# Kernel optimization log

Measured on AMD Instinct MI355X. Metric: run time of the kernel, lower is better.

The kernel has to match this reference:

```python
import jax, jax.numpy as jnp
import numpy as np

N, E, D, R = 100000, 1600000, 64, 16


def setup_inputs() -> dict:
    key = jax.random.key(0)
    k = jax.random.split(key, 8)
    feat = jax.random.normal(k[0], (N, D), dtype=jnp.float32)
    # xavier-uniform-ish scale (gain=sqrt(2), fan_in=fan_out=D) ~ std 0.177
    relation_weight = jax.random.normal(k[1], (R, D, D), dtype=jnp.float32) * 0.17
    relation_embed = jax.random.normal(k[2], (R, D), dtype=jnp.float32)
    W1 = jax.random.normal(k[3], (D, D), dtype=jnp.float32) * 0.1
    W2 = jax.random.normal(k[4], (D, D), dtype=jnp.float32) * 0.1
    src = jax.random.randint(k[5], (E,), 0, N, dtype=jnp.int32)
    dst = jax.random.randint(k[6], (E,), 0, N, dtype=jnp.int32)
    etype = jax.random.randint(k[7], (E,), 0, R, dtype=jnp.int32)
    return {"feat": feat, "relation_weight": relation_weight,
            "relation_embed": relation_embed, "W1": W1, "W2": W2,
            "src": src, "dst": dst, "etype": etype}


def reference(feat, relation_weight, relation_embed, W1, W2, src, dst, etype):
    n = feat.shape[0]
    # Project every node through every relation once ([N,R,D]) instead of
    # materializing the per-edge [E,D,D] weight gather; same math as
    # t_r = h_src @ W_{r(e)}, h_r = h_dst @ W_{r(e)}.
    proj = jnp.einsum('nd,rdo->nro', feat, relation_weight)  # [N,R,D]
    t_r = proj[src, etype]                                   # [E,D]
    h_r = proj[dst, etype]                                   # [E,D]
    # attention logit per edge: <t_r, tanh(h_r + r_embed)>
    att = jnp.sum(t_r * jnp.tanh(h_r + relation_embed[etype]), axis=-1)  # [E]
    # edge softmax over incoming edges of each destination node
    seg_max = jax.ops.segment_max(att, dst, num_segments=n)
    e = jnp.exp(att - seg_max[dst])
    seg_sum = jax.ops.segment_sum(e, dst, num_segments=n)
    a = e / seg_sum[dst]                                     # [E]
    # weighted aggregation of source features
    msgs = feat[src] * a[:, None]                            # [E,D]
    h_nb = jax.ops.segment_sum(msgs, dst, num_segments=n)    # [N,D]
    # Bi-interaction residual (torch leaky_relu default slope 0.01)
    out = (jax.nn.leaky_relu((feat + h_nb) @ W1.T, negative_slope=0.01)
           + jax.nn.leaky_relu((feat * h_nb) @ W2.T, negative_slope=0.01))
    return out
```

## Files before the change

kernel.cpp:

```cpp
#include <hip/hip_runtime.h>
#include <math.h>

#define D 64

typedef __attribute__((ext_vector_type(8))) short bf16x8;
typedef __attribute__((ext_vector_type(4))) float f32x4;
typedef __fp16 fp16x2 __attribute__((ext_vector_type(2)));

static __device__ __forceinline__ unsigned short f2bf(float f) {
    unsigned int u = __float_as_uint(f);
    unsigned int r = (u + 0x7FFFu + ((u >> 16) & 1u)) >> 16;
    return (unsigned short)r;
}
static __device__ __forceinline__ float bf2f(unsigned short h) {
    return __uint_as_float(((unsigned int)h) << 16);
}

#if defined(__has_builtin)
#if __has_builtin(__builtin_amdgcn_cvt_pk_bf16_f32)
#define HAVE_PK_BF16 1
#endif
#endif

static __device__ __forceinline__ unsigned int pk2bf(float a, float b) {
#ifdef HAVE_PK_BF16
    auto v = __builtin_amdgcn_cvt_pk_bf16_f32(a, b);
    return *(unsigned int*)&v;
#else
    return (unsigned int)f2bf(a) | ((unsigned int)f2bf(b) << 16);
#endif
}

static __device__ __forceinline__ unsigned int pk2h(float a, float b) {
    fp16x2 v = __builtin_amdgcn_cvt_pkrtz(a, b);
    return *(unsigned int*)&v;
}

static __device__ __forceinline__ float fast_tanh(float x) {
    float e = __expf(2.f * x);
    float r = __builtin_amdgcn_rcpf(e + 1.f);
    return 1.f - 2.f * r;
}

typedef __attribute__((address_space(1))) const unsigned int as1_uint;
typedef __attribute__((address_space(3))) unsigned int as3_uint;
static __device__ __forceinline__ void dma16(const void* g, void* l) {
    __builtin_amdgcn_global_load_lds((as1_uint*)g, (as3_uint*)l, 16, 0, 0);
}

static __device__ __forceinline__ int exscan_at(const int* __restrict__ tsc,
                                                const int* __restrict__ bofs, int i) {
    return (i == 0) ? 0 : (tsc[i - 1] + bofs[(i - 1) >> 10]);
}

__global__ __launch_bounds__(256) void k_prep(const float* __restrict__ W,
                                              unsigned short* __restrict__ B1h,
                                              unsigned short* __restrict__ B1l,
                                              unsigned short* __restrict__ B2h,
                                              unsigned short* __restrict__ B2l,
                                              const float* __restrict__ W1,
                                              const float* __restrict__ W2,
                                              unsigned short* __restrict__ F1h,
                                              unsigned short* __restrict__ F1l,
                                              unsigned short* __restrict__ F2h,
                                              unsigned short* __restrict__ F2l,
                                              const float* __restrict__ feat,
                                              unsigned short* __restrict__ fb,
                                              unsigned short* __restrict__ fh,
                                              unsigned short* __restrict__ fl,
                                              int R, int N) {
    int idx = blockIdx.x * 256 + threadIdx.x;
    const int nb = N * 16;
    const int nc = N * 8;
    if (idx < nb) {
        int n = idx >> 4, k = idx & 15;
        union { _Float16 h[4]; uint2 u; } cv;
        #pragma unroll
        for (int c = 0; c < 4; ++c)
            cv.h[c] = (_Float16)feat[(size_t)n * D + c * 16 + k];
        *(uint2*)&fb[(size_t)n * D + k * 4] = cv.u;
        return;
    }
    idx -= nb;
    if (idx < nc) {
        int n = idx >> 3, ch = idx & 7;
        const float* p = feat + (size_t)n * D + ch * 8;
        float4 v0 = *(const float4*)p, v1 = *(const float4*)(p + 4);
        float vals[8] = {v0.x, v0.y, v0.z, v0.w, v1.x, v1.y, v1.z, v1.w};
        bf16x8 hv, lv;
        #pragma unroll
        for (int j = 0; j < 8; ++j) {
            unsigned short h = f2bf(vals[j]);
            hv[j] = (short)h;
            lv[j] = (short)f2bf(vals[j] - bf2f(h));
        }
        *(bf16x8*)&fh[(size_t)n * D + ch * 8] = hv;
        *(bf16x8*)&fl[(size_t)n * D + ch * 8] = lv;
        return;
    }
    idx -= nc;
    int per_g = R * 512;
    if (idx < 2 * per_g) {
        int g = idx / per_g;
        int rest = idx % per_g;
        int r = rest >> 9;
        int rest2 = rest & 511;
        int c = rest2 >> 7;
        int kb = (rest2 >> 6) & 1;
        int lane = rest2 & 63;
        int m = lane & 15, q = lane >> 4;
        bf16x8 hv, lv;
        #pragma unroll
        for (int j = 0; j < 8; ++j) {
            float v;
            if (g == 0) v = W[(size_t)r * 4096 + (kb * 32 + q * 8 + j) * 64 + (c * 16 + m)];
            else        v = W[(size_t)r * 4096 + (c * 16 + m) * 64 + (kb * 32 + q * 8 + j)];
            unsigned short h = f2bf(v);
            hv[j] = (short)h;
            lv[j] = (short)f2bf(v - bf2f(h));
        }
        size_t off = ((((size_t)r * 4 + c) * 2 + kb) * 64 + lane) * 8;
        unsigned short* ph = (g == 0) ? B1h : B2h;
        unsigned short* pl = (g == 0) ? B1l : B2l;
        *(bf16x8*)&ph[off] = hv;
        *(bf16x8*)&pl[off] = lv;
    } else {
        int idx2 = idx - 2 * per_g;
        if (idx2 >= 1024) return;
        int g = idx2 >> 9;
        int rest2 = idx2 & 511;
        int c = rest2 >> 7;
        int kb = (rest2 >> 6) & 1;
        int lane = rest2 & 63;
        int m = lane & 15, q = lane >> 4;
        const float* Wx = g ? W2 : W1;
        bf16x8 hv, lv;
        #pragma unroll
        for (int j = 0; j < 8; ++j) {
            float v = Wx[(c * 16 + m) * 64 + kb * 32 + q * 8 + j];
            unsigned short h = f2bf(v);
            hv[j] = (short)h;
            lv[j] = (short)f2bf(v - bf2f(h));
        }
        size_t off = (((size_t)c * 2 + kb) * 64 + lane) * 8;
        unsigned short* ph = g ? F2h : F1h;
        unsigned short* pl = g ? F2l : F1l;
        *(bf16x8*)&ph[off] = hv;
        *(bf16x8*)&pl[off] = lv;
    }
}

#define NB3 256

__global__ __launch_bounds__(256) void k_bcount(const int* __restrict__ dst,
                                                int* __restrict__ cnt,
                                                int E, int CH, int NBUK) {
    __shared__ int h[1024];
    const int t = threadIdx.x, blk = blockIdx.x;
    for (int b = t; b < NBUK; b += 256) h[b] = 0;
    __syncthreads();
    const int s0 = blk * CH, s1 = min(E, s0 + CH);
    for (int e = s0 + t; e < s1; e += 256)
        atomicAdd(&h[dst[e] >> 7], 1);
    __syncthreads();
    for (int b = t; b < NBUK; b += 256)
        cnt[(b << 8) | blk] = h[b];
}

__global__ __launch_bounds__(256) void k_bscatter(const int* __restrict__ src,
                                                  const int* __restrict__ dst,
                                                  const int* __restrict__ etype,
                                                  const int* __restrict__ tsc,
                                                  const int* __restrict__ bofs,
                                                  int* __restrict__ ebuf,
                                                  int E, int CH, int NBUK) {
    __shared__ int cur[1024];
    const int t = threadIdx.x, blk = blockIdx.x;
    for (int b = t; b < NBUK; b += 256) cur[b] = exscan_at(tsc, bofs, (b << 8) | blk);
    __syncthreads();
    const int s0 = blk * CH, s1 = min(E, s0 + CH);
    for (int e = s0 + t; e < s1; e += 256) {
        int d = dst[e];
        int b = d >> 7;
        int pos = atomicAdd(&cur[b], 1);
        unsigned int pk = (unsigned int)src[e] | ((unsigned int)etype[e] << 20)
                        | ((unsigned int)(d & 127) << 25);
        ebuf[pos] = (int)pk;
    }
}

__global__ __launch_bounds__(256) void k_bcsr(const int* __restrict__ ebuf,
                                              const int* __restrict__ tsc,
                                              const int* __restrict__ bofs,
                                              int* __restrict__ offsets,
                                              int* __restrict__ spack,
                                              int N, int E, int NBUK) {
    __shared__ int sdeg[128], sincl[128], scur[128];
    const int t = threadIdx.x, b = blockIdx.x;
    const int s0 = exscan_at(tsc, bofs, b << 8);
    const int s1 = exscan_at(tsc, bofs, (b + 1) << 8);
    if (t < 128) { sdeg[t] = 0; }
    __syncthreads();
    for (int e = s0 + t; e < s1; e += 256)
        atomicAdd(&sdeg[((unsigned int)ebuf[e]) >> 25], 1);
    __syncthreads();
    if (t < 128) sincl[t] = sdeg[t];
    __syncthreads();
    for (int off = 1; off < 128; off <<= 1) {
        int v = 0;
        if (t < 128 && t >= off) v = sincl[t - off];
        __syncthreads();
        if (t < 128) sincl[t] += v;
        __syncthreads();
    }
    if (t < 128) {
        int excl = sincl[t] - sdeg[t];
        scur[t] = s0 + excl;
        int n = (b << 7) + t;
        if (n < N) offsets[n] = s0 + excl;
    }
    if (b == NBUK - 1 && t == 0) offsets[N] = E;
    __syncthreads();
    for (int e = s0 + t; e < s1; e += 256) {
        unsigned int pk = (unsigned int)ebuf[e];
        int i = pk >> 25;
        int p = atomicAdd(&scur[i], 1);
        spack[p] = (int)(pk & 0x01FFFFFFu);
    }
}

__global__ __launch_bounds__(1024) void k_scan1(const int* __restrict__ deg, int* __restrict__ tscan,
                                                int* __restrict__ bsum, int N) {
    __shared__ int s[1024];
    const int t = threadIdx.x;
    const int i = blockIdx.x * 1024 + t;
    int v = (i < N) ? deg[i] : 0;
    s[t] = v;
    __syncthreads();
    for (int off = 1; off < 1024; off <<= 1) {
        int tmp = (t >= off) ? s[t - off] : 0;
        __syncthreads();
        s[t] += tmp;
        __syncthreads();
    }
    if (i < N) tscan[i] = s[t];
    if (t == 1023) bsum[blockIdx.x] = s[1023];
}

__global__ __launch_bounds__(1024) void k_scan2(const int* __restrict__ bsum, int* __restrict__ bofs, int NB) {
    __shared__ int s[1024];
    const int t = threadIdx.x;
    int carry = 0;
    for (int b0 = 0; b0 < NB; b0 += 1024) {
        int i = b0 + t;
        int v = (i < NB) ? bsum[i] : 0;
        s[t] = v;
        __syncthreads();
        for (int off = 1; off < 1024; off <<= 1) {
            int tmp = (t >= off) ? s[t - off] : 0;
            __syncthreads();
            s[t] += tmp;
            __syncthreads();
        }
        if (i < NB) bofs[i] = carry + s[t] - v;
        int tot = s[1023];
        __syncthreads();
        carry += tot;
    }
}

__global__ __launch_bounds__(256, 4) void k_projv(const unsigned short* __restrict__ fh,
                                                  const unsigned short* __restrict__ fl,
                                                  const unsigned short* __restrict__ B1h,
                                                  const unsigned short* __restrict__ B1l,
                                                  const unsigned short* __restrict__ B2h,
                                                  const unsigned short* __restrict__ B2l,
                                                  const float* __restrict__ emb,
                                                  unsigned short* __restrict__ V,
                                                  int N, int R, int nrq) {
    const int tile = blockIdx.x / nrq;
    const int rq   = blockIdx.x % nrq;
    const int rbase = rq * 4;
    const int rcnt  = (R - rbase < 4) ? (R - rbase) : 4;
    const int n0 = tile * 128;
    __shared__ __align__(16) unsigned short Bbuf[32][512];
    __shared__ __align__(16) unsigned short Us[4][1024];
    const int t = threadIdx.x;
    const int lane = t & 63, w = t >> 6;
    const int m = lane & 15, q = lane >> 4;

    bf16x8 ah[2][2], al[2][2];
    #pragma unroll
    for (int s = 0; s < 2; ++s) {
        int n = n0 + w * 32 + s * 16 + m;
        bool ok = n < N;
        #pragma unroll
        for (int kb = 0; kb < 2; ++kb) {
            int d0 = kb * 32 + q * 8;
            if (ok) {
                ah[s][kb] = *(const bf16x8*)&fh[(size_t)n * D + d0];
                al[s][kb] = *(const bf16x8*)&fl[(size_t)n * D + d0];
            } else {
                #pragma unroll
                for (int j = 0; j < 8; ++j) { ah[s][kb][j] = 0; al[s][kb][j] = 0; }
            }
        }
    }

    auto stage_half = [&](int r, int half) {
        const unsigned short* arr = half ? ((w < 2) ? B2h : B2l)
                                         : ((w < 2) ? B1h : B1l);
        const unsigned short* gp = arr + (size_t)r * 4096 + (size_t)(w & 1) * 2048 + lane * 8;
        unsigned short* lp = &Bbuf[half * 16 + (w >> 1) * 8 + (w & 1) * 4][0];
        #pragma unroll
        for (int i = 0; i < 4; ++i)
            dma16(gp + i * 512, lp + i * 512);
    };

    stage_half(rbase, 0);
    stage_half(rbase, 1);
    __syncthreads();

    for (int rr = 0; rr < rcnt; ++rr) {
        const int r = rbase + rr;
        float em[4];
        #pragma unroll
        for (int c = 0; c < 4; ++c) em[c] = emb[r * 64 + c * 16 + m];

        f32x4 acc[4][2];
        #pragma unroll
        for (int c = 0; c < 4; ++c)
            #pragma unroll
            for (int s = 0; s < 2; ++s) acc[c][s] = (f32x4){0.f, 0.f, 0.f, 0.f};
        #pragma unroll
        for (int c = 0; c < 4; ++c) {
            bf16x8 bh[2], bl[2];
            #pragma unroll
            for (int kb = 0; kb < 2; ++kb) {
                bh[kb] = *(const bf16x8*)&Bbuf[c * 2 + kb][lane * 8];
                bl[kb] = *(const bf16x8*)&Bbuf[8 + c * 2 + kb][lane * 8];
            }
            #pragma unroll
            for (int s = 0; s < 2; ++s)
                #pragma unroll
                for (int kb = 0; kb < 2; ++kb) {
                    acc[c][s] = __builtin_amdgcn_mfma_f32_16x16x32_bf16(ah[s][kb], bh[kb], acc[c][s], 0, 0, 0);
                    acc[c][s] = __builtin_amdgcn_mfma_f32_16x16x32_bf16(al[s][kb], bh[kb], acc[c][s], 0, 0, 0);
                    acc[c][s] = __builtin_amdgcn_mfma_f32_16x16x32_bf16(ah[s][kb], bl[kb], acc[c][s], 0, 0, 0);
                }
        }

        __syncthreads();
        if (rr + 1 < rcnt) stage_half(r + 1, 0);

        #pragma unroll
        for (int s = 0; s < 2; ++s) {
            #pragma unroll
            for (int c = 0; c < 4; ++c) {
                int o = c * 16 + m;
                int kb2 = o >> 5;
                int q2 = (o >> 3) & 3;
                int j = o & 7;
                int Fb = kb2 * 64 + q2 * 16 + q * 4;
                #pragma unroll
                for (int i = 0; i < 4; i += 2) {
                    float t0 = fast_tanh(acc[c][s][i] + em[c]);
                    float t1 = fast_tanh(acc[c][s][i + 1] + em[c]);
                    unsigned int pk = pk2bf(t0, t1);
                    Us[w][((Fb + i) ^ q2) * 8 + j]     = (unsigned short)(pk & 0xFFFF);
                    Us[w][((Fb + i + 1) ^ q2) * 8 + j] = (unsigned short)(pk >> 16);
                }
            }

            bf16x8 ua[2];
            #pragma unroll
            for (int kb = 0; kb < 2; ++kb) {
                int F = kb * 64 + lane;
                ua[kb] = *(const bf16x8*)&Us[w][(F ^ (lane >> 4)) * 8];
            }
            f32x4 acc2[4];
            #pragma unroll
            for (int c = 0; c < 4; ++c) acc2[c] = (f32x4){0.f, 0.f, 0.f, 0.f};
            #pragma unroll
            for (int c = 0; c < 4; ++c) {
                bf16x8 bh[2], bl[2];
                #pragma unroll
                for (int kb = 0; kb < 2; ++kb) {
                    bh[kb] = *(const bf16x8*)&Bbuf[16 + c * 2 + kb][lane * 8];
                    bl[kb] = *(const bf16x8*)&Bbuf[24 + c * 2 + kb][lane * 8];
                }
                #pragma unroll
                for (int kb = 0; kb < 2; ++kb) {
                    acc2[c] = __builtin_amdgcn_mfma_f32_16x16x32_bf16(ua[kb], bh[kb], acc2[c], 0, 0, 0);
                    acc2[c] = __builtin_amdgcn_mfma_f32_16x16x32_bf16(ua[kb], bl[kb], acc2[c], 0, 0, 0);
                }
            }

            #pragma unroll
            for (int i = 0; i < 4; ++i) {
                int n = n0 + w * 32 + s * 16 + q * 4 + i;
                if (n < N) {
                    uint2 pv;
                    pv.x = pk2h(acc2[0][i], acc2[1][i]);
                    pv.y = pk2h(acc2[2][i], acc2[3][i]);
                    *(uint2*)&V[((size_t)n * R + r) * 64 + m * 4] = pv;
                }
            }
        }

        __syncthreads();
        if (rr + 1 < rcnt) stage_half(r + 1, 1);
    }
}

__global__ __launch_bounds__(256) void k_fused2(const unsigned short* __restrict__ V,
                                                const unsigned short* __restrict__ fb,
                                                const int* __restrict__ offsets,
                                                const int* __restrict__ spack,
                                                float* __restrict__ h_nb,
                                                int N, int R) {
    const int lane = threadIdx.x & 63;
    const int wav  = threadIdx.x >> 6;
    const int g    = lane >> 4;
    const int k    = lane & 15;
    const int n = blockIdx.x * 4 + wav;
    __shared__ __align__(16) unsigned short vlds[4][1024];

    if (n < N) {
        const unsigned short* gp = V + (size_t)n * 1024 + lane * 8;
        dma16(gp,       &vlds[wav][0]);
        dma16(gp + 512, &vlds[wav][512]);
    }
    __syncthreads();
    if (n >= N) return;

    const int beg = offsets[n], end = offsets[n + 1];
    float m = -INFINITY, l = 0.f;
    float4 acc = make_float4(0.f, 0.f, 0.f, 0.f);

    for (int cbeg = beg; cbeg < end; cbeg += 16) {
        float pv0, pv1, pv2, pv3;
        uint2 gv0, gv1, gv2, gv3;
        #pragma unroll
        for (int it = 0; it < 4; ++it) {
            int e = cbeg + it * 4 + g;
            bool ok = e < end;
            int pk = spack[ok ? e : end - 1];
            unsigned int off32 = (unsigned int)(pk & 0xFFFFF) * D + k * 4;
            uint2 fvu = *(const uint2*)&fb[off32];
            int et = pk >> 20;
            uint2 vvu = *(const uint2*)&vlds[wav][et * 64 + k * 4];
            union { uint2 u; fp16x2 h[2]; } cf, vv;
            cf.u = fvu; vv.u = vvu;
            float d = __builtin_amdgcn_fdot2(cf.h[0], vv.h[0], 0.f, false);
            d = __builtin_amdgcn_fdot2(cf.h[1], vv.h[1], d, false);
            d += __shfl_xor(d, 1, 64);
            d += __shfl_xor(d, 2, 64);
            d += __shfl_xor(d, 4, 64);
            d += __shfl_xor(d, 8, 64);
            d = ok ? d : -INFINITY;
            if (it == 0) { pv0 = d; gv0 = fvu; }
            else if (it == 1) { pv1 = d; gv1 = fvu; }
            else if (it == 2) { pv2 = d; gv2 = fvu; }
            else { pv3 = d; gv3 = fvu; }
        }
        float cm = fmaxf(fmaxf(pv0, pv1), fmaxf(pv2, pv3));
        cm = fmaxf(cm, __shfl_xor(cm, 16, 64));
        cm = fmaxf(cm, __shfl_xor(cm, 32, 64));
        float nm = fmaxf(m, cm);
        float scale = __expf(m - nm);
        float w0 = __expf(pv0 - nm);
        float w1 = __expf(pv1 - nm);
        float w2 = __expf(pv2 - nm);
        float w3 = __expf(pv3 - nm);
        float cs = w0 + w1 + w2 + w3;
        cs += __shfl_xor(cs, 16, 64);
        cs += __shfl_xor(cs, 32, 64);
        l = l * scale + cs;
        acc.x *= scale; acc.y *= scale; acc.z *= scale; acc.w *= scale;
        {
            union { uint2 u; _Float16 h[4]; } c0, c1, c2, c3;
            c0.u = gv0; c1.u = gv1; c2.u = gv2; c3.u = gv3;
            acc.x += w0 * (float)c0.h[0] + w1 * (float)c1.h[0]
                   + w2 * (float)c2.h[0] + w3 * (float)c3.h[0];
            acc.y += w0 * (float)c0.h[1] + w1 * (float)c1.h[1]
                   + w2 * (float)c2.h[1] + w3 * (float)c3.h[1];
            acc.z += w0 * (float)c0.h[2] + w1 * (float)c1.h[2]
                   + w2 * (float)c2.h[2] + w3 * (float)c3.h[2];
            acc.w += w0 * (float)c0.h[3] + w1 * (float)c1.h[3]
                   + w2 * (float)c2.h[3] + w3 * (float)c3.h[3];
        }
        m = nm;
    }

    acc.x += __shfl_xor(acc.x, 16, 64);
    acc.y += __shfl_xor(acc.y, 16, 64);
    acc.z += __shfl_xor(acc.z, 16, 64);
    acc.w += __shfl_xor(acc.w, 16, 64);
    acc.x += __shfl_xor(acc.x, 32, 64);
    acc.y += __shfl_xor(acc.y, 32, 64);
    acc.z += __shfl_xor(acc.z, 32, 64);
    acc.w += __shfl_xor(acc.w, 32, 64);
    float inv = (l != 0.f) ? 1.f / l : 0.f;
    if (lane < 16) {
        h_nb[(size_t)n * D + 0 * 16 + k] = acc.x * inv;
        h_nb[(size_t)n * D + 1 * 16 + k] = acc.y * inv;
        h_nb[(size_t)n * D + 2 * 16 + k] = acc.z * inv;
        h_nb[(size_t)n * D + 3 * 16 + k] = acc.w * inv;
    }
}

__global__ __launch_bounds__(256, 2) void k_final(const float* __restrict__ feat,
                                                  const float* __restrict__ h_nb,
                                                  const unsigned short* __restrict__ F1h,
                                                  const unsigned short* __restrict__ F1l,
                                                  const unsigned short* __restrict__ F2h,
                                                  const unsigned short* __restrict__ F2l,
                                                  float* __restrict__ out, int N) {
    const int n0 = blockIdx.x * 128;
    __shared__ __align__(16) unsigned short Wlds[4][4096];
    const int t = threadIdx.x;
    const int lane = t & 63, w = t >> 6;
    const int m = lane & 15, q = lane >> 4;

    const unsigned short* warr = (w == 0) ? F1h : (w == 1) ? F1l : (w == 2) ? F2h : F2l;
    #pragma unroll
    for (int i = 0; i < 8; ++i)
        dma16(warr + i * 512 + lane * 8, &Wlds[w][i * 512]);

    bf16x8 sh[2][2], sl[2][2], ph[2][2], pl[2][2];
    #pragma unroll
    for (int s = 0; s < 2; ++s) {
        int n = n0 + w * 32 + s * 16 + m;
        const float* fp = feat + (size_t)n * D;
        const float* hp = h_nb + (size_t)n * D;
        #pragma unroll
        for (int kb = 0; kb < 2; ++kb) {
            int d0 = kb * 32 + q * 8;
            float4 f0 = make_float4(0.f, 0.f, 0.f, 0.f), f1 = f0, h0 = f0, h1 = f0;
            if (n < N) {
                f0 = *(const float4*)(fp + d0); f1 = *(const float4*)(fp + d0 + 4);
                h0 = *(const float4*)(hp + d0); h1 = *(const float4*)(hp + d0 + 4);
            }
            float fv[8] = {f0.x, f0.y, f0.z, f0.w, f1.x, f1.y, f1.z, f1.w};
            float hv[8] = {h0.x, h0.y, h0.z, h0.w, h1.x, h1.y, h1.z, h1.w};
            bf16x8 a, b, c2, d2;
            #pragma unroll
            for (int j = 0; j < 8; ++j) {
                float xs = fv[j] + hv[j];
                float xp = fv[j] * hv[j];
                unsigned short hs = f2bf(xs);
                unsigned short hp2 = f2bf(xp);
                a[j]  = (short)hs;
                b[j]  = (short)f2bf(xs - bf2f(hs));
                c2[j] = (short)hp2;
                d2[j] = (short)f2bf(xp - bf2f(hp2));
            }
            sh[s][kb] = a; sl[s][kb] = b; ph[s][kb] = c2; pl[s][kb] = d2;
        }
    }
    __syncthreads();

    f32x4 a1[4][2], a2[4][2];
    #pragma unroll
    for (int c = 0; c < 4; ++c)
        #pragma unroll
        for (int s = 0; s < 2; ++s) {
            a1[c][s] = (f32x4){0.f, 0.f, 0.f, 0.f};
            a2[c][s] = (f32x4){0.f, 0.f, 0.f, 0.f};
        }
    #pragma unroll
    for (int c = 0; c < 4; ++c) {
        bf16x8 b1h[2], b1l[2], b2h[2], b2l[2];
        #pragma unroll
        for (int kb = 0; kb < 2; ++kb) {
            int o = (c * 2 + kb) * 512 + lane * 8;
            b1h[kb] = *(const bf16x8*)&Wlds[0][o];
            b1l[kb] = *(const bf16x8*)&Wlds[1][o];
            b2h[kb] = *(const bf16x8*)&Wlds[2][o];
            b2l[kb] = *(const bf16x8*)&Wlds[3][o];
        }
        #pragma unroll
        for (int kb = 0; kb < 2; ++kb)
            #pragma unroll
            for (int s = 0; s < 2; ++s) {
                a1[c][s] = __builtin_amdgcn_mfma_f32_16x16x32_bf16(sh[s][kb], b1h[kb], a1[c][s], 0, 0, 0);
                a1[c][s] = __builtin_amdgcn_mfma_f32_16x16x32_bf16(sl[s][kb], b1h[kb], a1[c][s], 0, 0, 0);
                a1[c][s] = __builtin_amdgcn_mfma_f32_16x16x32_bf16(sh[s][kb], b1l[kb], a1[c][s], 0, 0, 0);
                a2[c][s] = __builtin_amdgcn_mfma_f32_16x16x32_bf16(ph[s][kb], b2h[kb], a2[c][s], 0, 0, 0);
                a2[c][s] = __builtin_amdgcn_mfma_f32_16x16x32_bf16(pl[s][kb], b2h[kb], a2[c][s], 0, 0, 0);
                a2[c][s] = __builtin_amdgcn_mfma_f32_16x16x32_bf16(ph[s][kb], b2l[kb], a2[c][s], 0, 0, 0);
            }
    }

    #pragma unroll
    for (int s = 0; s < 2; ++s)
        #pragma unroll
        for (int i = 0; i < 4; ++i) {
            int n = n0 + w * 32 + s * 16 + q * 4 + i;
            if (n < N) {
                #pragma unroll
                for (int c = 0; c < 4; ++c) {
                    float o1 = a1[c][s][i];
                    float o2 = a2[c][s][i];
                    o1 = (o1 > 0.f) ? o1 : 0.01f * o1;
                    o2 = (o2 > 0.f) ? o2 : 0.01f * o2;
                    out[(size_t)n * D + c * 16 + m] = o1 + o2;
                }
            }
        }
}

extern "C" void kernel_launch(void* const* d_in, const int* in_sizes, int n_in,
                              void* d_out, int out_size, void* d_ws, size_t ws_size,
                              hipStream_t stream) {
    const float* feat  = (const float*)d_in[0];
    const float* relW  = (const float*)d_in[1];
    const float* relE  = (const float*)d_in[2];
    const float* W1    = (const float*)d_in[3];
    const float* W2    = (const float*)d_in[4];
    const int*   src   = (const int*)d_in[5];
    const int*   dst   = (const int*)d_in[6];
    const int*   etype = (const int*)d_in[7];
    float* out = (float*)d_out;

    const int N = in_sizes[0] / D;
    const int R = in_sizes[2] / D;
    const int E = in_sizes[5];

    char* w = (char*)d_ws;
    size_t off = 0;
    auto alloc = [&](size_t bytes) -> void* {
        void* p = w + off;
        off = (off + bytes + 255) & ~(size_t)255;
        return p;
    };
    unsigned short* varr = (unsigned short*)alloc((size_t)N * R * D * sizeof(unsigned short));
    float* h_nb   = (float*)alloc((size_t)N * D * sizeof(float));
    int* offsets  = (int*)alloc((size_t)(N + 1) * sizeof(int));
    int* bsum     = (int*)alloc(2048 * sizeof(int));
    int* bofs     = (int*)alloc(2048 * sizeof(int));
    int* spack    = (int*)alloc((size_t)E * sizeof(int));
    unsigned short* fb = (unsigned short*)alloc((size_t)N * D * sizeof(unsigned short));
    size_t wfrag = (size_t)R * 4 * 2 * 64 * 8;
    unsigned short* B1h = (unsigned short*)alloc(wfrag * sizeof(unsigned short));
    unsigned short* B1l = (unsigned short*)alloc(wfrag * sizeof(unsigned short));
    unsigned short* B2h = (unsigned short*)alloc(wfrag * sizeof(unsigned short));
    unsigned short* B2l = (unsigned short*)alloc(wfrag * sizeof(unsigned short));
    unsigned short* F1h = (unsigned short*)alloc(4096 * sizeof(unsigned short));
    unsigned short* F1l = (unsigned short*)alloc(4096 * sizeof(unsigned short));
    unsigned short* F2h = (unsigned short*)alloc(4096 * sizeof(unsigned short));
    unsigned short* F2l = (unsigned short*)alloc(4096 * sizeof(unsigned short));
    (void)ws_size; (void)n_in; (void)out_size;

    unsigned short* fh = (unsigned short*)h_nb;
    unsigned short* fl = fh + (size_t)N * D;

    const int NBUK = (N + 127) >> 7;
    const int CH   = (E + NB3 - 1) / NB3;
    const int L    = NBUK << 8;
    int* ebuf = (int*)varr;
    int* cnt  = ebuf + E;
    int* tsc  = cnt + L;
    const int NBscan = (L + 1023) / 1024;

    const int nrq = (R + 3) / 4;
    const int ntiles = (N + 127) / 128;
    const int nPrep = N * 16 + N * 8 + 2 * R * 512 + 1024;

    k_prep<<<(nPrep + 255) / 256, 256, 0, stream>>>(relW, B1h, B1l, B2h, B2l,
                                                    W1, W2, F1h, F1l, F2h, F2l,
                                                    feat, fb, fh, fl, R, N);
    k_bcount<<<NB3, 256, 0, stream>>>(dst, cnt, E, CH, NBUK);
    k_scan1<<<NBscan, 1024, 0, stream>>>(cnt, tsc, bsum, L);
    k_scan2<<<1, 1024, 0, stream>>>(bsum, bofs, NBscan);
    k_bscatter<<<NB3, 256, 0, stream>>>(src, dst, etype, tsc, bofs, ebuf, E, CH, NBUK);
    k_bcsr<<<NBUK, 256, 0, stream>>>(ebuf, tsc, bofs, offsets, spack, N, E, NBUK);
    k_projv<<<ntiles * nrq, 256, 0, stream>>>(fh, fl, B1h, B1l, B2h, B2l, relE, varr, N, R, nrq);
    k_fused2<<<(N + 3) / 4, 256, 0, stream>>>(varr, fb, offsets, spack, h_nb, N, R);
    k_final<<<(N + 127) / 128, 256, 0, stream>>>(feat, h_nb, F1h, F1l, F2h, F2l, out, N);
}
```

Before: 345.3 us.

## Fuse bucket count into prep, drop scan2, restructure edge aggregation lanes

The bucket-count kernel is merged into the prep kernel as extra blocks, and the second-level scan kernel is removed: each scatter and CSR block now rebuilds the block-offset prefix from bsum in shared memory. The fused attention/aggregation kernel is reworked so that each lane handles one edge and a 16-channel slice (16 edges per wave), using 16-byte loads and fewer shuffles. It rescales the accumulator only when the running max changes and reduces partial sums across edges through LDS. This cuts kernel launches and shuffle traffic in exchange for redundant per-block scans and more registers and LDS per thread.

```diff
diff --git a/kernel.cpp b/kernel.cpp
--- a/kernel.cpp
+++ b/kernel.cpp
@@ -46,11 +46,6 @@
 typedef __attribute__((address_space(3))) unsigned int as3_uint;
 static __device__ __forceinline__ void dma16(const void* g, void* l) {
     __builtin_amdgcn_global_load_lds((as1_uint*)g, (as3_uint*)l, 16, 0, 0);
-}
-
-static __device__ __forceinline__ int exscan_at(const int* __restrict__ tsc,
-                                                const int* __restrict__ bofs, int i) {
-    return (i == 0) ? 0 : (tsc[i - 1] + bofs[(i - 1) >> 10]);
 }
 
 __global__ __launch_bounds__(256) void k_prep(const float* __restrict__ W,
@@ -68,7 +63,23 @@
                                               unsigned short* __restrict__ fb,
                                               unsigned short* __restrict__ fh,
                                               unsigned short* __restrict__ fl,
-                                              int R, int N) {
+                                              const int* __restrict__ dst,
+                                              int* __restrict__ cnt,
+                                              int R, int N, int E, int CH,
+                                              int NBUK, int PB) {
+    if ((int)blockIdx.x >= PB) {
+        __shared__ int h[1024];
+        const int t = threadIdx.x, blk = blockIdx.x - PB;
+        for (int b = t; b < NBUK; b += 256) h[b] = 0;
+        __syncthreads();
+        const int s0 = blk * CH, s1 = min(E, s0 + CH);
+        for (int e = s0 + t; e < s1; e += 256)
+            atomicAdd(&h[dst[e] >> 7], 1);
+        __syncthreads();
+        for (int b = t; b < NBUK; b += 256)
+            cnt[(b << 8) | blk] = h[b];
+        return;
+    }
     int idx = blockIdx.x * 256 + threadIdx.x;
     const int nb = N * 16;
     const int nc = N * 8;
@@ -152,31 +163,56 @@
 
 #define NB3 256
 
-__global__ __launch_bounds__(256) void k_bcount(const int* __restrict__ dst,
-                                                int* __restrict__ cnt,
-                                                int E, int CH, int NBUK) {
-    __shared__ int h[1024];
-    const int t = threadIdx.x, blk = blockIdx.x;
-    for (int b = t; b < NBUK; b += 256) h[b] = 0;
-    __syncthreads();
-    const int s0 = blk * CH, s1 = min(E, s0 + CH);
-    for (int e = s0 + t; e < s1; e += 256)
-        atomicAdd(&h[dst[e] >> 7], 1);
-    __syncthreads();
-    for (int b = t; b < NBUK; b += 256)
-        cnt[(b << 8) | blk] = h[b];
+__global__ __launch_bounds__(1024) void k_scan1(const int* __restrict__ deg, int* __restrict__ tscan,
+                                                int* __restrict__ bsum, int N) {
+    __shared__ int s[1024];
+    const int t = threadIdx.x;
+    const int i = blockIdx.x * 1024 + t;
+    int v = (i < N) ? deg[i] : 0;
+    s[t] = v;
+    __syncthreads();
+    for (int off = 1; off < 1024; off <<= 1) {
+        int tmp = (t >= off) ? s[t - off] : 0;
+        __syncthreads();
+        s[t] += tmp;
+        __syncthreads();
+    }
+    if (i < N) tscan[i] = s[t];
+    if (t == 1023) bsum[blockIdx.x] = s[1023];
+}
+
+static __device__ __forceinline__ void build_sbp(const int* __restrict__ bsum,
+                                                 int* ss, int* sbp, int NBS) {
+    const int t = threadIdx.x;
+    int v = (t < NBS) ? bsum[t] : 0;
+    ss[t] = v;
+    __syncthreads();
+    for (int off = 1; off < 256; off <<= 1) {
+        int tmp = (t >= off) ? ss[t - off] : 0;
+        __syncthreads();
+        ss[t] += tmp;
+        __syncthreads();
+    }
+    sbp[t] = ss[t] - v;
+    __syncthreads();
 }
 
 __global__ __launch_bounds__(256) void k_bscatter(const int* __restrict__ src,
                                                   const int* __restrict__ dst,
                                                   const int* __restrict__ etype,
                                                   const int* __restrict__ tsc,
-                                                  const int* __restrict__ bofs,
+                                                  const int* __restrict__ bsum,
                                                   int* __restrict__ ebuf,
-                                                  int E, int CH, int NBUK) {
+                                                  int E, int CH, int NBUK, int NBS) {
     __shared__ int cur[1024];
+    __shared__ int ss[256];
+    __shared__ int sbp[256];
     const int t = threadIdx.x, blk = blockIdx.x;
-    for (int b = t; b < NBUK; b += 256) cur[b] = exscan_at(tsc, bofs, (b << 8) | blk);
+    build_sbp(bsum, ss, sbp, NBS);
+    for (int b = t; b < NBUK; b += 256) {
+        int i = (b << 8) | blk;
+        cur[b] = (i == 0) ? 0 : (tsc[i - 1] + sbp[(i - 1) >> 10]);
+    }
     __syncthreads();
     const int s0 = blk * CH, s1 = min(E, s0 + CH);
     for (int e = s0 + t; e < s1; e += 256) {
@@ -191,14 +227,19 @@
 
 __global__ __launch_bounds__(256) void k_bcsr(const int* __restrict__ ebuf,
                                               const int* __restrict__ tsc,
-                                              const int* __restrict__ bofs,
+                                              const int* __restrict__ bsum,
                                               int* __restrict__ offsets,
                                               int* __restrict__ spack,
-                                              int N, int E, int NBUK) {
+                                              int N, int E, int NBUK, int NBS) {
     __shared__ int sdeg[128], sincl[128], scur[128];
+    __shared__ int ss[256];
+    __shared__ int sbp[256];
     const int t = threadIdx.x, b = blockIdx.x;
-    const int s0 = exscan_at(tsc, bofs, b << 8);
-    const int s1 = exscan_at(tsc, bofs, (b + 1) << 8);
+    build_sbp(bsum, ss, sbp, NBS);
+    int i0 = b << 8;
+    int i1 = (b + 1) << 8;
+    const int s0 = (i0 == 0) ? 0 : (tsc[i0 - 1] + sbp[(i0 - 1) >> 10]);
+    const int s1 = tsc[i1 - 1] + sbp[(i1 - 1) >> 10];
     if (t < 128) { sdeg[t] = 0; }
     __syncthreads();
     for (int e = s0 + t; e < s1; e += 256)
@@ -226,46 +267,6 @@
         int i = pk >> 25;
         int p = atomicAdd(&scur[i], 1);
         spack[p] = (int)(pk & 0x01FFFFFFu);
-    }
-}
-
-__global__ __launch_bounds__(1024) void k_scan1(const int* __restrict__ deg, int* __restrict__ tscan,
-                                                int* __restrict__ bsum, int N) {
-    __shared__ int s[1024];
-    const int t = threadIdx.x;
-    const int i = blockIdx.x * 1024 + t;
-    int v = (i < N) ? deg[i] : 0;
-    s[t] = v;
-    __syncthreads();
-    for (int off = 1; off < 1024; off <<= 1) {
-        int tmp = (t >= off) ? s[t - off] : 0;
-        __syncthreads();
-        s[t] += tmp;
-        __syncthreads();
-    }
-    if (i < N) tscan[i] = s[t];
-    if (t == 1023) bsum[blockIdx.x] = s[1023];
-}
-
-__global__ __launch_bounds__(1024) void k_scan2(const int* __restrict__ bsum, int* __restrict__ bofs, int NB) {
-    __shared__ int s[1024];
-    const int t = threadIdx.x;
-    int carry = 0;
-    for (int b0 = 0; b0 < NB; b0 += 1024) {
-        int i = b0 + t;
-        int v = (i < NB) ? bsum[i] : 0;
-        s[t] = v;
-        __syncthreads();
-        for (int off = 1; off < 1024; off <<= 1) {
-            int tmp = (t >= off) ? s[t - off] : 0;
-            __syncthreads();
-            s[t] += tmp;
-            __syncthreads();
-        }
-        if (i < NB) bofs[i] = carry + s[t] - v;
-        int tot = s[1023];
-        __syncthreads();
-        carry += tot;
     }
 }
 
@@ -421,10 +422,11 @@
                                                 int N, int R) {
     const int lane = threadIdx.x & 63;
     const int wav  = threadIdx.x >> 6;
-    const int g    = lane >> 4;
-    const int k    = lane & 15;
+    const int ei   = lane >> 2;
+    const int sub  = lane & 3;
     const int n = blockIdx.x * 4 + wav;
     __shared__ __align__(16) unsigned short vlds[4][1024];
+    __shared__ __align__(16) float rlds[4][64 * 20];
 
     if (n < N) {
         const unsigned short* gp = V + (size_t)n * 1024 + lane * 8;
@@ -436,78 +438,70 @@
 
     const int beg = offsets[n], end = offsets[n + 1];
     float m = -INFINITY, l = 0.f;
-    float4 acc = make_float4(0.f, 0.f, 0.f, 0.f);
+    float acc[16];
+    #pragma unroll
+    for (int i = 0; i < 16; ++i) acc[i] = 0.f;
 
     for (int cbeg = beg; cbeg < end; cbeg += 16) {
-        float pv0, pv1, pv2, pv3;
-        uint2 gv0, gv1, gv2, gv3;
-        #pragma unroll
-        for (int it = 0; it < 4; ++it) {
-            int e = cbeg + it * 4 + g;
-            bool ok = e < end;
-            int pk = spack[ok ? e : end - 1];
-            unsigned int off32 = (unsigned int)(pk & 0xFFFFF) * D + k * 4;
-            uint2 fvu = *(const uint2*)&fb[off32];
-            int et = pk >> 20;
-            uint2 vvu = *(const uint2*)&vlds[wav][et * 64 + k * 4];
-            union { uint2 u; fp16x2 h[2]; } cf, vv;
-            cf.u = fvu; vv.u = vvu;
-            float d = __builtin_amdgcn_fdot2(cf.h[0], vv.h[0], 0.f, false);
-            d = __builtin_amdgcn_fdot2(cf.h[1], vv.h[1], d, false);
-            d += __shfl_xor(d, 1, 64);
-            d += __shfl_xor(d, 2, 64);
-            d += __shfl_xor(d, 4, 64);
-            d += __shfl_xor(d, 8, 64);
-            d = ok ? d : -INFINITY;
-            if (it == 0) { pv0 = d; gv0 = fvu; }
-            else if (it == 1) { pv1 = d; gv1 = fvu; }
-            else if (it == 2) { pv2 = d; gv2 = fvu; }
-            else { pv3 = d; gv3 = fvu; }
-        }
-        float cm = fmaxf(fmaxf(pv0, pv1), fmaxf(pv2, pv3));
+        int e = cbeg + ei;
+        bool ok = e < end;
+        int pk = spack[ok ? e : end - 1];
+        unsigned int fo = (unsigned int)(pk & 0xFFFFF) * D + sub * 16;
+        int et = pk >> 20;
+        union { uint4 u[2]; fp16x2 h2[8]; _Float16 s[16]; } cf, vv;
+        cf.u[0] = *(const uint4*)&fb[fo];
+        cf.u[1] = *(const uint4*)&fb[fo + 8];
+        vv.u[0] = *(const uint4*)&vlds[wav][et * 64 + sub * 16];
+        vv.u[1] = *(const uint4*)&vlds[wav][et * 64 + sub * 16 + 8];
+        float d0 = __builtin_amdgcn_fdot2(cf.h2[0], vv.h2[0], 0.f, false);
+        d0 = __builtin_amdgcn_fdot2(cf.h2[1], vv.h2[1], d0, false);
+        d0 = __builtin_amdgcn_fdot2(cf.h2[2], vv.h2[2], d0, false);
+        d0 = __builtin_amdgcn_fdot2(cf.h2[3], vv.h2[3], d0, false);
+        float d1 = __builtin_amdgcn_fdot2(cf.h2[4], vv.h2[4], 0.f, false);
+        d1 = __builtin_amdgcn_fdot2(cf.h2[5], vv.h2[5], d1, false);
+        d1 = __builtin_amdgcn_fdot2(cf.h2[6], vv.h2[6], d1, false);
+        d1 = __builtin_amdgcn_fdot2(cf.h2[7], vv.h2[7], d1, false);
+        float d = d0 + d1;
+        d += __shfl_xor(d, 1, 64);
+        d += __shfl_xor(d, 2, 64);
+        d = ok ? d : -INFINITY;
+        float cm = fmaxf(d, __shfl_xor(d, 4, 64));
+        cm = fmaxf(cm, __shfl_xor(cm, 8, 64));
         cm = fmaxf(cm, __shfl_xor(cm, 16, 64));
         cm = fmaxf(cm, __shfl_xor(cm, 32, 64));
         float nm = fmaxf(m, cm);
-        float scale = __expf(m - nm);
-        float w0 = __expf(pv0 - nm);
-        float w1 = __expf(pv1 - nm);
-        float w2 = __expf(pv2 - nm);
-        float w3 = __expf(pv3 - nm);
-        float cs = w0 + w1 + w2 + w3;
+        float wgt = __expf(d - nm);
+        float cs = wgt + __shfl_xor(wgt, 4, 64);
+        cs += __shfl_xor(cs, 8, 64);
         cs += __shfl_xor(cs, 16, 64);
         cs += __shfl_xor(cs, 32, 64);
-        l = l * scale + cs;
-        acc.x *= scale; acc.y *= scale; acc.z *= scale; acc.w *= scale;
-        {
-            union { uint2 u; _Float16 h[4]; } c0, c1, c2, c3;
-            c0.u = gv0; c1.u = gv1; c2.u = gv2; c3.u = gv3;
-            acc.x += w0 * (float)c0.h[0] + w1 * (float)c1.h[0]
-                   + w2 * (float)c2.h[0] + w3 * (float)c3.h[0];
-            acc.y += w0 * (float)c0.h[1] + w1 * (float)c1.h[1]
-                   + w2 * (float)c2.h[1] + w3 * (float)c3.h[1];
-            acc.z += w0 * (float)c0.h[2] + w1 * (float)c1.h[2]
-                   + w2 * (float)c2.h[2] + w3 * (float)c3.h[2];
-            acc.w += w0 * (float)c0.h[3] + w1 * (float)c1.h[3]
-                   + w2 * (float)c2.h[3] + w3 * (float)c3.h[3];
-        }
-        m = nm;
-    }
-
-    acc.x += __shfl_xor(acc.x, 16, 64);
-    acc.y += __shfl_xor(acc.y, 16, 64);
-    acc.z += __shfl_xor(acc.z, 16, 64);
-    acc.w += __shfl_xor(acc.w, 16, 64);
-    acc.x += __shfl_xor(acc.x, 32, 64);
-    acc.y += __shfl_xor(acc.y, 32, 64);
-    acc.z += __shfl_xor(acc.z, 32, 64);
-    acc.w += __shfl_xor(acc.w, 32, 64);
+        if (nm != m) {
+            float scale = __expf(m - nm);
+            l *= scale;
+            #pragma unroll
+            for (int i = 0; i < 16; ++i) acc[i] *= scale;
+            m = nm;
+        }
+        l += cs;
+        #pragma unroll
+        for (int i = 0; i < 16; ++i)
+            acc[i] += wgt * (float)cf.s[i];
+    }
+
+    #pragma unroll
+    for (int i = 0; i < 16; ++i) {
+        int ch = (i & 3) * 16 + sub * 4 + (i >> 2);
+        rlds[wav][ch * 20 + ei] = acc[i];
+    }
+    const float* row = &rlds[wav][lane * 20];
+    float4 r0 = *(const float4*)row;
+    float4 r1 = *(const float4*)(row + 4);
+    float4 r2 = *(const float4*)(row + 8);
+    float4 r3 = *(const float4*)(row + 12);
+    float s = ((r0.x + r0.y) + (r0.z + r0.w)) + ((r1.x + r1.y) + (r1.z + r1.w))
+            + ((r2.x + r2.y) + (r2.z + r2.w)) + ((r3.x + r3.y) + (r3.z + r3.w));
     float inv = (l != 0.f) ? 1.f / l : 0.f;
-    if (lane < 16) {
-        h_nb[(size_t)n * D + 0 * 16 + k] = acc.x * inv;
-        h_nb[(size_t)n * D + 1 * 16 + k] = acc.y * inv;
-        h_nb[(size_t)n * D + 2 * 16 + k] = acc.z * inv;
-        h_nb[(size_t)n * D + 3 * 16 + k] = acc.w * inv;
-    }
+    h_nb[(size_t)n * D + lane] = s * inv;
 }
 
 __global__ __launch_bounds__(256, 2) void k_final(const float* __restrict__ feat,
@@ -639,7 +633,6 @@
     float* h_nb   = (float*)alloc((size_t)N * D * sizeof(float));
     int* offsets  = (int*)alloc((size_t)(N + 1) * sizeof(int));
     int* bsum     = (int*)alloc(2048 * sizeof(int));
-    int* bofs     = (int*)alloc(2048 * sizeof(int));
     int* spack    = (int*)alloc((size_t)E * sizeof(int));
     unsigned short* fb = (unsigned short*)alloc((size_t)N * D * sizeof(unsigned short));
     size_t wfrag = (size_t)R * 4 * 2 * 64 * 8;
@@ -667,15 +660,15 @@
     const int nrq = (R + 3) / 4;
     const int ntiles = (N + 127) / 128;
     const int nPrep = N * 16 + N * 8 + 2 * R * 512 + 1024;
-
-    k_prep<<<(nPrep + 255) / 256, 256, 0, stream>>>(relW, B1h, B1l, B2h, B2l,
-                                                    W1, W2, F1h, F1l, F2h, F2l,
-                                                    feat, fb, fh, fl, R, N);
-    k_bcount<<<NB3, 256, 0, stream>>>(dst, cnt, E, CH, NBUK);
+    const int PB = (nPrep + 255) / 256;
+
+    k_prep<<<PB + NB3, 256, 0, stream>>>(relW, B1h, B1l, B2h, B2l,
+                                         W1, W2, F1h, F1l, F2h, F2l,
+                                         feat, fb, fh, fl,
+                                         dst, cnt, R, N, E, CH, NBUK, PB);
     k_scan1<<<NBscan, 1024, 0, stream>>>(cnt, tsc, bsum, L);
-    k_scan2<<<1, 1024, 0, stream>>>(bsum, bofs, NBscan);
-    k_bscatter<<<NB3, 256, 0, stream>>>(src, dst, etype, tsc, bofs, ebuf, E, CH, NBUK);
-    k_bcsr<<<NBUK, 256, 0, stream>>>(ebuf, tsc, bofs, offsets, spack, N, E, NBUK);
+    k_bscatter<<<NB3, 256, 0, stream>>>(src, dst, etype, tsc, bsum, ebuf, E, CH, NBUK, NBscan);
+    k_bcsr<<<NBUK, 256, 0, stream>>>(ebuf, tsc, bsum, offsets, spack, N, E, NBUK, NBscan);
     k_projv<<<ntiles * nrq, 256, 0, stream>>>(fh, fl, B1h, B1l, B2h, B2l, relE, varr, N, R, nrq);
     k_fused2<<<(N + 3) / 4, 256, 0, stream>>>(varr, fb, offsets, spack, h_nb, N, R);
     k_final<<<(N + 127) / 128, 256, 0, stream>>>(feat, h_nb, F1h, F1l, F2h, F2l, out, N);
```

Result: slower. 357.5 us (+3.5%).
